# Optimization experiments

Measured on AMD Instinct MI355X. Metric: run time of the kernel, lower is better.

The kernel has to match this reference:

```python
import jax, jax.numpy as jnp
import numpy as np

BATCH = 4096
D_IN = 8192
D_OUT = 8192
B = 128            # block size
K_IN = D_IN // B   # 64 (D_IN divisible by B -> no padding)
K_OUT = D_OUT // B # 64 (D_OUT divisible by B -> no trailing slice)
INIT_SCALE = 0.1


def setup_inputs() -> dict:
    key = jax.random.key(0)
    kx, kw, kd = jax.random.split(key, 3)
    x = jax.random.normal(kx, (BATCH, D_IN), dtype=jnp.float32)
    W = jax.random.normal(kw, (K_OUT, K_IN, B), dtype=jnp.float32) * INIT_SCALE
    # Bernoulli +/-1 diagonal signs over input dims
    D = jnp.where(jax.random.bernoulli(kd, p=0.5, shape=(D_IN,)), 1.0, -1.0).astype(jnp.float32)
    return {"x": x, "W": W, "D": D}


def reference(x, W, D):
    # x: (batch, d_in); W: (k_out, k_in, b) first rows of circulant blocks; D: (d_in,) signs
    batch = x.shape[0]
    k_out, k_in, b = W.shape
    x_blocks = (x * D[None, :]).reshape(batch, k_in, b)  # d_in divisible by b -> no pad
    # Batched FFT of all input blocks and all weight first-rows at once
    Xf = jnp.fft.fft(x_blocks, axis=-1)          # (batch, k_in, b) complex
    Wf = jnp.conj(jnp.fft.fft(W, axis=-1))       # (k_out, k_in, b) complex
    # Sum over k_in in the frequency domain: per-frequency complex contraction
    Yf = jnp.einsum('bji,oji->boi', Xf, Wf)      # (batch, k_out, b)
    out = jnp.fft.ifft(Yf, axis=-1).real         # (batch, k_out, b)
    return out.reshape(batch, k_out * b)         # k_out*b == d_out -> no slice
```

## Files before the change

### kernel.cpp

```cpp
#include <hip/hip_runtime.h>


typedef __bf16 bf16;
typedef __bf16 bf16x8 __attribute__((ext_vector_type(8)));
typedef float f32x4 __attribute__((ext_vector_type(4)));

#define PI_F 3.14159265358979323846f

#define WS_B1   0u
#define WS_B2T  49152u
#define WS_WMAT 90112u
#define WS_X    2220032u

__device__ __forceinline__ unsigned int pack_bf2(float a, float b) {
    unsigned short ra = __builtin_bit_cast(unsigned short, (bf16)a);
    unsigned short rb = __builtin_bit_cast(unsigned short, (bf16)b);
    return (unsigned int)ra | ((unsigned int)rb << 16);
}

__global__ __launch_bounds__(256) void init_basis(bf16* __restrict__ B1,
                                                  bf16* __restrict__ B2T) {
    int gid = blockIdx.x * 256 + threadIdx.x;
    if (gid < 192 * 128) {
        int fc = gid >> 7, t = gid & 127;
        int f = fc >> 1;
        float v = 0.f;
        if (f <= 64) {
            int a = (f * t) & 127;
            float ang = a * (PI_F / 64.f);
            v = (fc & 1) ? -__sinf(ang) : __cosf(ang);
        }
        B1[gid] = (bf16)v;
    }
    if (gid < 128 * 160) {
        int t = gid / 160, fc = gid % 160;
        int f = fc >> 1, c = fc & 1;
        float v = 0.f;
        if (f == 0) {
            v = c ? 0.f : (1.f / 128.f);
        } else if (f == 64) {
            v = c ? 0.f : ((t & 1) ? -1.f / 128.f : 1.f / 128.f);
        } else if (f < 64) {
            int a = (f * t) & 127;
            float ang = a * (PI_F / 64.f);
            v = c ? (-2.f / 128.f) * __sinf(ang) : (2.f / 128.f) * __cosf(ang);
        }
        B2T[gid] = (bf16)v;
    }
}

__global__ __launch_bounds__(256) void init_wmat(const float* __restrict__ W,
                                                 bf16* __restrict__ Wm) {
    __shared__ float ct[128], st[128];
    const int tid = threadIdx.x;
    if (tid < 128) {
        float ang = tid * (PI_F / 64.f);
        ct[tid] = __cosf(ang);
        st[tid] = __sinf(ang);
    }
    __syncthreads();
    int gid = blockIdx.x * 256 + tid;
    if (gid >= 65 * 4096) return;
    int f = gid >> 12;
    int rem = gid & 4095;
    int o = rem >> 6, j = rem & 63;
    const float* wp = W + (((o << 6) + j) << 7);
    float wr = 0.f, wi = 0.f;
    for (int tau = 0; tau < 128; tau++) {
        float w = wp[tau];
        int a = (f * tau) & 127;
        wr += w * ct[a];
        wi += w * st[a];
    }
    bf16* base = Wm + ((size_t)f * 128 + 2 * o) * 128 + 2 * j;
    base[0]   = (bf16)wr;
    base[1]   = (bf16)(-wi);
    base[128] = (bf16)wi;
    base[129] = (bf16)wr;
}

__global__ __launch_bounds__(256) void k1_dft(const float* __restrict__ x,
                                              const float* __restrict__ D,
                                              const bf16* __restrict__ B1,
                                              bf16* __restrict__ X) {
    __shared__ bf16 xs[8][16][136];
    const int tid = threadIdx.x;
    const int wave = tid >> 6, lane = tid & 63;
    const int q = lane >> 4, nl = lane & 15;
    const int s_t = blockIdx.x >> 1, jh = blockIdx.x & 1;
    const int s0 = s_t * 16;

    bf16x8 bfrag[3][4];
#pragma unroll
    for (int t = 0; t < 3; t++) {
        int nt = wave + 4 * t;
#pragma unroll
        for (int kc = 0; kc < 4; kc++)
            bfrag[t][kc] = *(const bf16x8*)(B1 + (nt * 16 + nl) * 128 + kc * 32 + q * 8);
    }

    for (int grp = 0; grp < 4; grp++) {
        const int jb = jh * 32 + grp * 8;
        __syncthreads();
        {
            const int jl = tid >> 5, ss = (tid >> 1) & 15, th = tid & 1;
            const float* xp = x + (size_t)(s0 + ss) * 8192 + (jb + jl) * 128 + th * 64;
            const float* Dp = D + (jb + jl) * 128 + th * 64;
            bf16* dst = &xs[jl][ss][th * 64];
#pragma unroll
            for (int u = 0; u < 8; u++) {
                float4 a  = *(const float4*)(xp + u * 8);
                float4 b  = *(const float4*)(xp + u * 8 + 4);
                float4 da = *(const float4*)(Dp + u * 8);
                float4 db = *(const float4*)(Dp + u * 8 + 4);
                bf16x8 o;
                o[0] = (bf16)(a.x * da.x); o[1] = (bf16)(a.y * da.y);
                o[2] = (bf16)(a.z * da.z); o[3] = (bf16)(a.w * da.w);
                o[4] = (bf16)(b.x * db.x); o[5] = (bf16)(b.y * db.y);
                o[6] = (bf16)(b.z * db.z); o[7] = (bf16)(b.w * db.w);
                *(bf16x8*)(dst + u * 8) = o;
            }
        }
        __syncthreads();

        f32x4 acc[3][8];
        const f32x4 zero = {0.f, 0.f, 0.f, 0.f};
#pragma unroll
        for (int t = 0; t < 3; t++)
#pragma unroll
            for (int j = 0; j < 8; j++) acc[t][j] = zero;

#pragma unroll
        for (int j = 0; j < 8; j++) {
#pragma unroll
            for (int kc = 0; kc < 4; kc++) {
                bf16x8 a = *(const bf16x8*)&xs[j][nl][kc * 32 + q * 8];
#pragma unroll
                for (int t = 0; t < 3; t++)
                    acc[t][j] = __builtin_amdgcn_mfma_f32_16x16x32_bf16(
                        a, bfrag[t][kc], acc[t][j], 0, 0, 0);
            }
        }

        const int par = lane & 1;
#pragma unroll
        for (int t = 0; t < 3; t++) {
            const int fc = (wave + 4 * t) * 16 + nl;
            const int fpr = fc >> 1;
            const bool wr = (fc < 130);
#pragma unroll
            for (int r = 0; r < 4; r++) {
                float sh[8];
#pragma unroll
                for (int j = 0; j < 8; j++)
                    sh[j] = __shfl_xor(acc[t][j][r], 1);
                unsigned int d0, d1, d2, d3;
                if (!par) {
                    d0 = pack_bf2(acc[t][0][r], sh[0]);
                    d1 = pack_bf2(acc[t][1][r], sh[1]);
                    d2 = pack_bf2(acc[t][2][r], sh[2]);
                    d3 = pack_bf2(acc[t][3][r], sh[3]);
                } else {
                    d0 = pack_bf2(sh[4], acc[t][4][r]);
                    d1 = pack_bf2(sh[5], acc[t][5][r]);
                    d2 = pack_bf2(sh[6], acc[t][6][r]);
                    d3 = pack_bf2(sh[7], acc[t][7][r]);
                }
                if (wr) {
                    char* p = (char*)X + ((size_t)fpr * 4096 + s0 + q * 4 + r) * 256
                              + jb * 4 + par * 16;
                    *(uint4*)p = make_uint4(d0, d1, d2, d3);
                }
            }
        }
    }
}

__global__ __launch_bounds__(256) void k2_gemm(const bf16* __restrict__ X,
                                               const bf16* __restrict__ Wmat,
                                               const bf16* __restrict__ B2T,
                                               float* __restrict__ out) {
    __shared__ bf16 ybuf[8 * 16 * 136 + 32];
    const int tid = threadIdx.x;
    const int wave = tid >> 6, lane = tid & 63;
    const int q = lane >> 4, nl = lane & 15;
    const int s_t = blockIdx.x >> 3, o_t = blockIdx.x & 7;
    const int s0 = s_t * 16;

    {
        unsigned int* yz = (unsigned int*)ybuf;
        for (int i = tid; i < (8 * 16 * 136 + 32) / 2; i += 256) yz[i] = 0u;
    }
    __syncthreads();

    for (int grp = 0; grp < 17; grp++) {
        const int f = grp * 4 + wave;
        if (f < 65) {
            f32x4 acc = {0.f, 0.f, 0.f, 0.f};
#pragma unroll
            for (int kc = 0; kc < 4; kc++) {
                bf16x8 a = *(const bf16x8*)(Wmat + ((size_t)f * 128 + o_t * 16 + nl) * 128
                                            + kc * 32 + q * 8);
                bf16x8 b = *(const bf16x8*)(X + ((size_t)f * 4096 + s0 + nl) * 128
                                            + kc * 32 + q * 8);
                acc = __builtin_amdgcn_mfma_f32_16x16x32_bf16(a, b, acc, 0, 0, 0);
            }
#pragma unroll
            for (int r = 0; r < 4; r++) {
                int oc = q * 4 + r;
                int o = oc >> 1, c = oc & 1;
                ybuf[(o * 16 + nl) * 136 + 2 * f + c] = (bf16)acc[r];
            }
        }
    }
    __syncthreads();

    for (int p = wave; p < 64; p += 4) {
        const int o = p >> 3, nt = p & 7;
        f32x4 acc = {0.f, 0.f, 0.f, 0.f};
#pragma unroll
        for (int kc = 0; kc < 5; kc++) {
            bf16x8 a = *(const bf16x8*)&ybuf[(o * 16 + nl) * 136 + kc * 32 + q * 8];
            bf16x8 b = *(const bf16x8*)(B2T + (nt * 16 + nl) * 160 + kc * 32 + q * 8);
            acc = __builtin_amdgcn_mfma_f32_16x16x32_bf16(a, b, acc, 0, 0, 0);
        }
        float* op = out + (size_t)(s0 + q * 4) * 8192 + (o_t * 8 + o) * 128 + nt * 16 + nl;
#pragma unroll
        for (int r = 0; r < 4; r++)
            op[(size_t)r * 8192] = acc[r];
    }
}

extern "C" void kernel_launch(void* const* d_in, const int* in_sizes, int n_in,
                              void* d_out, int out_size, void* d_ws, size_t ws_size,
                              hipStream_t stream) {
    const float* x = (const float*)d_in[0];
    const float* W = (const float*)d_in[1];
    const float* D = (const float*)d_in[2];
    float* out = (float*)d_out;
    char* ws = (char*)d_ws;
    bf16* B1  = (bf16*)(ws + WS_B1);
    bf16* B2T = (bf16*)(ws + WS_B2T);
    bf16* Wm  = (bf16*)(ws + WS_WMAT);
    bf16* X   = (bf16*)(ws + WS_X);

    hipLaunchKernelGGL(init_basis, dim3(96), dim3(256), 0, stream, B1, B2T);
    hipLaunchKernelGGL(init_wmat, dim3(1040), dim3(256), 0, stream, W, Wm);
    hipLaunchKernelGGL(k1_dft, dim3(512), dim3(256), 0, stream, x, D, B1, X);
    hipLaunchKernelGGL(k2_gemm, dim3(2048), dim3(256), 0, stream, X, Wm, B2T, out);
}
```

Before: 465.1 us.

## Split fused frequency GEMM and inverse DFT into two kernels via workspace

Replaces the fused k2_gemm with two kernels. k2a_freq does the per-frequency complex contraction with weights staged in shared memory and writes an intermediate Y in bf16 to the workspace. k2b_idft then applies the inverse DFT as a dense MFMA GEMM. Separately, init_wmat now runs one block per output row and caches W in shared memory, and the k1 x-load is recoded for coalesced float4 reads. The split costs an extra round trip of roughly 84MB through global memory and depends on the workspace being large enough, otherwise it falls back to the old kernel.

```diff
diff --git a/kernel.cpp b/kernel.cpp
--- a/kernel.cpp
+++ b/kernel.cpp
@@ -2,6 +2,7 @@
 
 
 typedef __bf16 bf16;
+typedef __bf16 bf16x4 __attribute__((ext_vector_type(4)));
 typedef __bf16 bf16x8 __attribute__((ext_vector_type(8)));
 typedef float f32x4 __attribute__((ext_vector_type(4)));
 
@@ -11,6 +12,8 @@
 #define WS_B2T  49152u
 #define WS_WMAT 90112u
 #define WS_X    2220032u
+#define WS_Y    70377472ull
+#define WS_NEED 154263552ull
 
 __device__ __forceinline__ unsigned int pack_bf2(float a, float b) {
     unsigned short ra = __builtin_bit_cast(unsigned short, (bf16)a);
@@ -51,32 +54,40 @@
 
 __global__ __launch_bounds__(256) void init_wmat(const float* __restrict__ W,
                                                  bf16* __restrict__ Wm) {
+    __shared__ float wrow[64 * 129];
     __shared__ float ct[128], st[128];
     const int tid = threadIdx.x;
+    const int o = blockIdx.x;
     if (tid < 128) {
         float ang = tid * (PI_F / 64.f);
         ct[tid] = __cosf(ang);
         st[tid] = __sinf(ang);
     }
-    __syncthreads();
-    int gid = blockIdx.x * 256 + tid;
-    if (gid >= 65 * 4096) return;
-    int f = gid >> 12;
-    int rem = gid & 4095;
-    int o = rem >> 6, j = rem & 63;
-    const float* wp = W + (((o << 6) + j) << 7);
-    float wr = 0.f, wi = 0.f;
-    for (int tau = 0; tau < 128; tau++) {
-        float w = wp[tau];
-        int a = (f * tau) & 127;
-        wr += w * ct[a];
-        wi += w * st[a];
-    }
-    bf16* base = Wm + ((size_t)f * 128 + 2 * o) * 128 + 2 * j;
-    base[0]   = (bf16)wr;
-    base[1]   = (bf16)(-wi);
-    base[128] = (bf16)wi;
-    base[129] = (bf16)wr;
+    for (int i = tid; i < 2048; i += 256) {
+        float4 v = *(const float4*)(W + (size_t)o * 8192 + i * 4);
+        int j = i >> 5, c = i & 31;
+        float* d = &wrow[j * 129 + c * 4];
+        d[0] = v.x; d[1] = v.y; d[2] = v.z; d[3] = v.w;
+    }
+    __syncthreads();
+    const int j = tid & 63, fq = tid >> 6;
+    for (int fo = 0; fo < 17; fo++) {
+        int f = fo * 4 + fq;
+        if (f > 64) continue;
+        float wr = 0.f, wi = 0.f;
+        int a = 0;
+        for (int tau = 0; tau < 128; tau++) {
+            float w = wrow[j * 129 + tau];
+            wr += w * ct[a];
+            wi += w * st[a];
+            a = (a + f) & 127;
+        }
+        bf16* base = Wm + ((size_t)f * 128 + 2 * o) * 128 + 2 * j;
+        base[0]   = (bf16)wr;
+        base[1]   = (bf16)(-wi);
+        base[128] = (bf16)wi;
+        base[129] = (bf16)wr;
+    }
 }
 
 __global__ __launch_bounds__(256) void k1_dft(const float* __restrict__ x,
@@ -103,22 +114,19 @@
         const int jb = jh * 32 + grp * 8;
         __syncthreads();
         {
-            const int jl = tid >> 5, ss = (tid >> 1) & 15, th = tid & 1;
-            const float* xp = x + (size_t)(s0 + ss) * 8192 + (jb + jl) * 128 + th * 64;
-            const float* Dp = D + (jb + jl) * 128 + th * 64;
-            bf16* dst = &xs[jl][ss][th * 64];
-#pragma unroll
-            for (int u = 0; u < 8; u++) {
-                float4 a  = *(const float4*)(xp + u * 8);
-                float4 b  = *(const float4*)(xp + u * 8 + 4);
-                float4 da = *(const float4*)(Dp + u * 8);
-                float4 db = *(const float4*)(Dp + u * 8 + 4);
-                bf16x8 o;
-                o[0] = (bf16)(a.x * da.x); o[1] = (bf16)(a.y * da.y);
-                o[2] = (bf16)(a.z * da.z); o[3] = (bf16)(a.w * da.w);
-                o[4] = (bf16)(b.x * db.x); o[5] = (bf16)(b.y * db.y);
-                o[6] = (bf16)(b.z * db.z); o[7] = (bf16)(b.w * db.w);
-                *(bf16x8*)(dst + u * 8) = o;
+            const int l32 = tid & 31;
+#pragma unroll
+            for (int it = 0; it < 16; ++it) {
+                int seg = it * 8 + (tid >> 5);
+                int jl = seg >> 4, ss = seg & 15;
+                const float* xp = x + (size_t)(s0 + ss) * 8192 + (jb + jl) * 128 + l32 * 4;
+                const float* dp = D + (jb + jl) * 128 + l32 * 4;
+                float4 a = *(const float4*)xp;
+                float4 d = *(const float4*)dp;
+                bf16x4 ov;
+                ov[0] = (bf16)(a.x * d.x); ov[1] = (bf16)(a.y * d.y);
+                ov[2] = (bf16)(a.z * d.z); ov[3] = (bf16)(a.w * d.w);
+                *(bf16x4*)&xs[jl][ss][l32 * 4] = ov;
             }
         }
         __syncthreads();
@@ -176,6 +184,133 @@
     }
 }
 
+__global__ __launch_bounds__(256) void k2a_freq(const bf16* __restrict__ X,
+                                                const bf16* __restrict__ Wmat,
+                                                bf16* __restrict__ Y) {
+    __shared__ bf16 sA[128 * 136];
+    const int tid = threadIdx.x;
+    const int wave = tid >> 6, lane = tid & 63;
+    const int q = lane >> 4, nl = lane & 15;
+    const int b = blockIdx.x;
+    const int s_t = b & 31, oc_t = (b >> 5) & 3, fg = b >> 7;
+    const int oc0 = oc_t * 32;
+    const int sbase = s_t * 128 + wave * 32;
+
+#pragma unroll
+    for (int it = 0; it < 8; ++it) {
+        int i = it * 256 + tid;
+        int row = i >> 4, pos = i & 15;
+        int f = fg * 4 + (row >> 5);
+        if (f < 65) {
+            *(uint4*)&sA[row * 136 + pos * 8] =
+                *(const uint4*)(Wmat + ((size_t)f * 128 + oc0 + (row & 31)) * 128 + pos * 8);
+        }
+    }
+    __syncthreads();
+
+    f32x4 acc[4][2][2];
+    const f32x4 zero = {0.f, 0.f, 0.f, 0.f};
+#pragma unroll
+    for (int F = 0; F < 4; F++)
+#pragma unroll
+        for (int m = 0; m < 2; m++)
+#pragma unroll
+            for (int n = 0; n < 2; n++) acc[F][m][n] = zero;
+
+#pragma unroll
+    for (int F = 0; F < 4; F++) {
+        const int f = fg * 4 + F;
+        if (f < 65) {
+#pragma unroll
+            for (int kc = 0; kc < 4; kc++) {
+                bf16x8 bfr[2];
+#pragma unroll
+                for (int n = 0; n < 2; n++)
+                    bfr[n] = *(const bf16x8*)(X + ((size_t)f * 4096 + sbase + n * 16 + nl) * 128
+                                              + kc * 32 + q * 8);
+#pragma unroll
+                for (int m = 0; m < 2; m++) {
+                    bf16x8 afr = *(const bf16x8*)&sA[(F * 32 + m * 16 + nl) * 136 + kc * 32 + q * 8];
+#pragma unroll
+                    for (int n = 0; n < 2; n++)
+                        acc[F][m][n] = __builtin_amdgcn_mfma_f32_16x16x32_bf16(
+                            afr, bfr[n], acc[F][m][n], 0, 0, 0);
+                }
+            }
+        }
+    }
+
+#pragma unroll
+    for (int m = 0; m < 2; m++) {
+#pragma unroll
+        for (int n = 0; n < 2; n++) {
+            const int s = sbase + n * 16 + nl;
+#pragma unroll
+            for (int p = 0; p < 2; p++) {
+                const int o = oc_t * 16 + m * 8 + q * 2 + p;
+                bf16x8 v;
+#pragma unroll
+                for (int F = 0; F < 4; F++) {
+                    v[2 * F]     = (bf16)acc[F][m][n][2 * p];
+                    v[2 * F + 1] = (bf16)acc[F][m][n][2 * p + 1];
+                }
+                *(bf16x8*)(Y + ((size_t)s * 64 + o) * 160 + fg * 8) = v;
+            }
+        }
+    }
+}
+
+__global__ __launch_bounds__(256) void k2b_idft(const bf16* __restrict__ Y,
+                                                const bf16* __restrict__ B2T,
+                                                float* __restrict__ out) {
+    __shared__ bf16 sB[128 * 168];
+    const int tid = threadIdx.x;
+    const int wave = tid >> 6, lane = tid & 63;
+    const int q = lane >> 4, nl = lane & 15;
+    const size_t r0 = (size_t)blockIdx.x * 256;
+
+    for (int i = tid; i < 2560; i += 256) {
+        int row = i / 20, pos = i - row * 20;
+        *(uint4*)&sB[row * 168 + pos * 8] = *(const uint4*)(B2T + row * 160 + pos * 8);
+    }
+    __syncthreads();
+
+    f32x4 acc[4][8];
+    const f32x4 zero = {0.f, 0.f, 0.f, 0.f};
+#pragma unroll
+    for (int m = 0; m < 4; m++)
+#pragma unroll
+        for (int n = 0; n < 8; n++) acc[m][n] = zero;
+
+    const size_t rbase = r0 + wave * 64 + nl;
+#pragma unroll
+    for (int kc = 0; kc < 5; kc++) {
+        bf16x8 af[4];
+#pragma unroll
+        for (int m = 0; m < 4; m++)
+            af[m] = *(const bf16x8*)(Y + (rbase + m * 16) * 160 + kc * 32 + q * 8);
+#pragma unroll
+        for (int n = 0; n < 8; n++) {
+            bf16x8 bf = *(const bf16x8*)&sB[(n * 16 + nl) * 168 + kc * 32 + q * 8];
+#pragma unroll
+            for (int m = 0; m < 4; m++)
+                acc[m][n] = __builtin_amdgcn_mfma_f32_16x16x32_bf16(af[m], bf, acc[m][n], 0, 0, 0);
+        }
+    }
+
+#pragma unroll
+    for (int m = 0; m < 4; m++) {
+        const size_t row = r0 + wave * 64 + m * 16 + q * 4;
+#pragma unroll
+        for (int n = 0; n < 8; n++) {
+            float* op = out + row * 128 + n * 16 + nl;
+#pragma unroll
+            for (int r = 0; r < 4; r++)
+                op[(size_t)r * 128] = acc[m][n][r];
+        }
+    }
+}
+
 __global__ __launch_bounds__(256) void k2_gemm(const bf16* __restrict__ X,
                                                const bf16* __restrict__ Wmat,
                                                const bf16* __restrict__ B2T,
@@ -243,9 +378,15 @@
     bf16* B2T = (bf16*)(ws + WS_B2T);
     bf16* Wm  = (bf16*)(ws + WS_WMAT);
     bf16* X   = (bf16*)(ws + WS_X);
+    bf16* Y   = (bf16*)(ws + WS_Y);
 
     hipLaunchKernelGGL(init_basis, dim3(96), dim3(256), 0, stream, B1, B2T);
-    hipLaunchKernelGGL(init_wmat, dim3(1040), dim3(256), 0, stream, W, Wm);
+    hipLaunchKernelGGL(init_wmat, dim3(64), dim3(256), 0, stream, W, Wm);
     hipLaunchKernelGGL(k1_dft, dim3(512), dim3(256), 0, stream, x, D, B1, X);
-    hipLaunchKernelGGL(k2_gemm, dim3(2048), dim3(256), 0, stream, X, Wm, B2T, out);
-}
+    if (ws_size >= WS_NEED) {
+        hipLaunchKernelGGL(k2a_freq, dim3(2176), dim3(256), 0, stream, X, Wm, Y);
+        hipLaunchKernelGGL(k2b_idft, dim3(1024), dim3(256), 0, stream, Y, B2T, out);
+    } else {
+        hipLaunchKernelGGL(k2_gemm, dim3(2048), dim3(256), 0, stream, X, Wm, B2T, out);
+    }
+}
```

Result: no change. 466.8 us (+0.4%).
